# Kernel tuning notes

Measured on AMD Instinct MI355X. Metric: run time of the kernel, lower is better.

The kernel has to match this reference:

```python
import jax, jax.numpy as jnp
import numpy as np

H = 512      # hidden_size
NH = 8       # num_heads
DH = H // NH # head_dim = 64
NL = 2       # num_layers
R = 64       # number of AST relation types
PAD = 0      # padding relation index
FF = 4 * H   # FFN inner dim
B, T, S = 4, 512, 512
NEG = -1e10
EPS = 1e-5


def layer_norm(x, g, b):
    m = jnp.mean(x, axis=-1, keepdims=True)
    v = jnp.mean((x - m) ** 2, axis=-1, keepdims=True)
    return (x - m) * jax.lax.rsqrt(v + EPS) * g + b


def setup_inputs() -> dict:
    key = jax.random.key(0)
    ks = iter(jax.random.split(key, 40))

    def n(shape, scale=0.02):
        return jax.random.normal(next(ks), shape, dtype=jnp.float32) * scale

    inp = {
        'q': jax.random.normal(next(ks), (B, T, H), dtype=jnp.float32),
        'kv': jax.random.normal(next(ks), (B, S, H), dtype=jnp.float32),
        'rel_emb_k': n((R, DH)).at[PAD].set(0.0),
        'rel_emb_v': n((R, DH)).at[PAD].set(0.0),
        'Wq_s': n((NL, H, H)), 'bq_s': jnp.zeros((NL, H)),
        'Wk_s': n((NL, H, H)), 'Wv_s': n((NL, H, H)),
        'Wo_s': n((NL, H, H)), 'bo_s': jnp.zeros((NL, H)),
        'ln1_g': jnp.ones((NL, H)), 'ln1_b': jnp.zeros((NL, H)),
        'Wq_c': n((NL, H, H)), 'bq_c': jnp.zeros((NL, H)),
        'Wk_c': n((NL, H, H)), 'Wv_c': n((NL, H, H)),
        'Wo_c': n((NL, H, H)), 'bo_c': jnp.zeros((NL, H)),
        'ln2_g': jnp.ones((NL, H)), 'ln2_b': jnp.zeros((NL, H)),
        'W1': n((NL, H, FF)), 'b1': jnp.zeros((NL, FF)),
        'W2': n((NL, FF, H)), 'b2': jnp.zeros((NL, H)),
        'ln3_g': jnp.ones((NL, H)), 'ln3_b': jnp.zeros((NL, H)),
        'rel_ids': jax.random.randint(next(ks), (B, T, T), 0, R),
        'enc_mask': jnp.ones((B, S), dtype=bool),
    }
    return inp


def reference(q, kv, rel_emb_k, rel_emb_v,
              Wq_s, bq_s, Wk_s, Wv_s, Wo_s, bo_s, ln1_g, ln1_b,
              Wq_c, bq_c, Wk_c, Wv_c, Wo_c, bo_c, ln2_g, ln2_b,
              W1, b1, W2, b2, ln3_g, ln3_b,
              rel_ids, enc_mask):
    scale = np.sqrt(DH).astype(np.float32)
    # relation embeddings shared across layers/heads: [B,T,T,DH]
    rel_k = rel_emb_k[rel_ids]
    rel_v = rel_emb_v[rel_ids]
    tril = jnp.tril(jnp.ones((T, T), dtype=bool))
    rel_mask = (rel_ids != PAD) & tril[None]

    o = q
    for i in range(NL):
        # --- relation-aware masked self-attention ---
        Q = (o @ Wq_s[i] + bq_s[i]).reshape(B, T, NH, DH)
        K = (o @ Wk_s[i]).reshape(B, T, NH, DH)
        V = (o @ Wv_s[i]).reshape(B, T, NH, DH)
        # Q . (K + rel_k)^T decomposed to avoid materializing [B,NH,T,T,DH]
        e = (jnp.einsum('blhd,bmhd->bhlm', Q, K)
             + jnp.einsum('blhd,blmd->bhlm', Q, rel_k)) / scale
        e = jnp.where(rel_mask[:, None], e, NEG)
        a = jax.nn.softmax(e, axis=-1)
        att = (jnp.einsum('bhlm,bmhd->blhd', a, V)
               + jnp.einsum('bhlm,blmd->blhd', a, rel_v)).reshape(B, T, H)
        o = layer_norm(o + att @ Wo_s[i] + bo_s[i], ln1_g[i], ln1_b[i])

        # --- cross-attention ---
        Qc = (o @ Wq_c[i] + bq_c[i]).reshape(B, T, NH, DH)
        Kc = (kv @ Wk_c[i]).reshape(B, S, NH, DH)
        Vc = (kv @ Wv_c[i]).reshape(B, S, NH, DH)
        ec = jnp.einsum('bthd,bshd->bhts', Qc, Kc) / scale
        ec = jnp.where(enc_mask[:, None, None, :], ec, NEG)
        ac = jax.nn.softmax(ec, axis=-1)
        oc = jnp.einsum('bhts,bshd->bthd', ac, Vc).reshape(B, T, H)
        o = layer_norm(o + oc @ Wo_c[i] + bo_c[i], ln2_g[i], ln2_b[i])

        # --- feedforward ---
        h = jax.nn.relu(o @ W1[i] + b1[i])
        o = layer_norm(o + h @ W2[i] + b2[i], ln3_g[i], ln3_b[i])
    return o
```

## Files before the change

kernel.cpp:

```cpp
#include <hip/hip_runtime.h>

static constexpr int Hc  = 512;
static constexpr int NHc = 8;
static constexpr int DHc = 64;
static constexpr int NLc = 2;
static constexpr int Rc  = 64;
static constexpr int FFc = 2048;
static constexpr int Bc  = 4;
static constexpr int Tc  = 512;
#define NEGV (-1e10f)
#define EPSV 1e-5f
#define THRV 6.0f

typedef unsigned short u16;
typedef unsigned char u8;
typedef __attribute__((ext_vector_type(8))) short s16x8;
typedef __attribute__((ext_vector_type(4))) float f32x4;

__device__ __forceinline__ f32x4 mfma_bf16(s16x8 a, s16x8 b, f32x4 c) {
  return __builtin_amdgcn_mfma_f32_16x16x32_bf16(a, b, c, 0, 0, 0);
}
__device__ __forceinline__ u16 f2bf(float f) {
  union { float f; unsigned u; } x; x.f = f;
  unsigned r = (x.u + 0x7FFFu + ((x.u >> 16) & 1u)) >> 16;
  return (u16)r;
}
__device__ __forceinline__ float bf2f(u16 h) {
  union { unsigned u; float f; } x; x.u = ((unsigned)h) << 16;
  return x.f;
}
__device__ __forceinline__ unsigned cvtpk(float a, float b) {
  unsigned r;
  asm("v_cvt_pk_bf16_f32 %0, %1, %2" : "=v"(r) : "v"(a), "v"(b));
  return r;
}

template <int BM, int BN, bool RELU, int OUT>
__global__ __launch_bounds__(256) void gemm_mfma(
    const u16* __restrict__ A, const u16* __restrict__ Wt,
    const float* __restrict__ bias, int biasN,
    void* __restrict__ Cout, int N, int K) {
  __shared__ u16 As[BM * 32];
  __shared__ u16 Bs[BN * 32];
  const int tid = threadIdx.x;
  const int w = tid >> 6, lane = tid & 63, g = lane >> 4, li = lane & 15;
  const int bn = blockIdx.x * BN, bm = blockIdx.y * BM;
  const int r0 = (w & 1) * (BM / 2), c0 = (w >> 1) * (BN / 2);
  constexpr int MR = BM / 32, NR = BN / 32;
  constexpr int AIT = BM / 64, BIT = BN / 64;
  f32x4 acc[MR][NR];
#pragma unroll
  for (int i = 0; i < MR; ++i)
#pragma unroll
    for (int j = 0; j < NR; ++j) acc[i][j] = (f32x4){0.f, 0.f, 0.f, 0.f};

  s16x8 va[AIT], vb[BIT];
#pragma unroll
  for (int it = 0; it < AIT; ++it) {
    int s = it * 256 + tid, row = s >> 2, ch = s & 3;
    va[it] = *(const s16x8*)(A + (size_t)(bm + row) * K + ch * 8);
  }
#pragma unroll
  for (int it = 0; it < BIT; ++it) {
    int s = it * 256 + tid, row = s >> 2, ch = s & 3;
    vb[it] = *(const s16x8*)(Wt + (size_t)(bn + row) * K + ch * 8);
  }

  for (int k0 = 0; k0 < K; k0 += 32) {
    __syncthreads();
#pragma unroll
    for (int it = 0; it < AIT; ++it) {
      int s = it * 256 + tid, row = s >> 2, ch = s & 3;
      *(s16x8*)&As[row * 32 + ((ch ^ (row & 3)) * 8)] = va[it];
    }
#pragma unroll
    for (int it = 0; it < BIT; ++it) {
      int s = it * 256 + tid, row = s >> 2, ch = s & 3;
      *(s16x8*)&Bs[row * 32 + ((ch ^ (row & 3)) * 8)] = vb[it];
    }
    if (k0 + 32 < K) {
#pragma unroll
      for (int it = 0; it < AIT; ++it) {
        int s = it * 256 + tid, row = s >> 2, ch = s & 3;
        va[it] = *(const s16x8*)(A + (size_t)(bm + row) * K + k0 + 32 + ch * 8);
      }
#pragma unroll
      for (int it = 0; it < BIT; ++it) {
        int s = it * 256 + tid, row = s >> 2, ch = s & 3;
        vb[it] = *(const s16x8*)(Wt + (size_t)(bn + row) * K + k0 + 32 + ch * 8);
      }
    }
    __syncthreads();
    s16x8 ar[MR], br[NR];
#pragma unroll
    for (int i = 0; i < MR; ++i) {
      int row = r0 + i * 16 + li;
      ar[i] = *(const s16x8*)&As[row * 32 + ((g ^ (row & 3)) * 8)];
    }
#pragma unroll
    for (int j = 0; j < NR; ++j) {
      int row = c0 + j * 16 + li;
      br[j] = *(const s16x8*)&Bs[row * 32 + ((g ^ (row & 3)) * 8)];
    }
#pragma unroll
    for (int i = 0; i < MR; ++i)
#pragma unroll
      for (int j = 0; j < NR; ++j) acc[i][j] = mfma_bf16(ar[i], br[j], acc[i][j]);
  }

#pragma unroll
  for (int j = 0; j < NR; ++j) {
    int col = bn + c0 + j * 16 + li;
    float bv = (bias && col < biasN) ? bias[col] : 0.f;
#pragma unroll
    for (int i = 0; i < MR; ++i) {
#pragma unroll
      for (int r = 0; r < 4; ++r) {
        int rowg = bm + r0 + i * 16 + 4 * g + r;
        float v = acc[i][j][r] + bv;
        if (RELU) v = fmaxf(v, 0.f);
        if (OUT == 0) ((float*)Cout)[(size_t)rowg * N + col] = v;
        else          ((u16*)Cout)[(size_t)rowg * N + col] = f2bf(v);
      }
    }
  }
}

struct WPtrs { const float* p[10]; };

__global__ __launch_bounds__(256) void wcvt(WPtrs wp, u16* __restrict__ dst) {
  constexpr int NE = 20;
  constexpr int srcIdx[NE] = {0,1,0,1,3,3,4,4,5,5,6,6,7,7,2,2,8,8,9,9};
  constexpr int srcOff[NE] = {0,0,262144,262144,0,262144,0,262144,0,262144,
                              0,262144,0,262144,0,262144,0,1048576,0,1048576};
  constexpr int dstOff[NE] = {0,262144,524288,786432,1048576,1310720,
                              1572864,1835008,2097152,2359296,2621440,2883584,
                              3145728,3407872,3670016,3932160,
                              4194304,5242880,6291456,7340032};
  constexpr int KsA[NE] = {512,512,512,512,512,512,512,512,512,512,
                           512,512,512,512,512,512,512,512,2048,2048};
  constexpr int NsA[NE] = {512,512,512,512,512,512,512,512,512,512,
                           512,512,512,512,512,512,2048,2048,512,512};
  constexpr int tileStart[NE] = {0,64,128,192,256,320,384,448,512,576,
                                 640,704,768,832,896,960,1024,1280,1536,1792};
  __shared__ float ts[64 * 65];
  const int tid = threadIdx.x;
  const int bid = blockIdx.x;
  int e = 0;
#pragma unroll
  for (int i = 1; i < NE; ++i) if (bid >= tileStart[i]) e = i;
  const int t = bid - tileStart[e];
  const int Ks_ = KsA[e], Ns_ = NsA[e];
  const int tn = t % (Ns_ >> 6), tk = t / (Ns_ >> 6);
  const float* src = wp.p[srcIdx[e]] + srcOff[e];

  {
    int r = tid >> 2, cb = (tid & 3) * 16;
    const float* sp = src + (size_t)(tk * 64 + r) * Ns_ + tn * 64 + cb;
#pragma unroll
    for (int j = 0; j < 4; ++j) {
      float4 v = ((const float4*)sp)[j];
      float* d = &ts[r * 65 + cb + j * 4];
      d[0] = v.x; d[1] = v.y; d[2] = v.z; d[3] = v.w;
    }
  }
  __syncthreads();
  {
    int n = tid >> 2, kb = (tid & 3) * 16;
    u16* dp = dst + dstOff[e] + (size_t)(tn * 64 + n) * Ks_ + tk * 64 + kb;
    s16x8 o0, o1;
#pragma unroll
    for (int j = 0; j < 8; ++j) o0[j] = (short)f2bf(ts[(kb + j) * 65 + n]);
#pragma unroll
    for (int j = 0; j < 8; ++j) o1[j] = (short)f2bf(ts[(kb + 8 + j) * 65 + n]);
    *(s16x8*)dp = o0;
    *(s16x8*)(dp + 8) = o1;
  }
}

__global__ __launch_bounds__(256) void acvt(
    const float* __restrict__ q, const float* __restrict__ kv,
    const float* __restrict__ relv, const int* __restrict__ rel,
    u16* __restrict__ obf, u16* __restrict__ kvbf, u16* __restrict__ relvt,
    u8* __restrict__ rel8, float* __restrict__ ocp) {
  int bid = blockIdx.x, tid = threadIdx.x;
  if (bid >= 1025) {
    size_t i = (size_t)(bid - 1025) * 2048 + (size_t)tid * 8;
    int4 a = *(const int4*)(rel + i);
    int4 b = *(const int4*)(rel + i + 4);
    unsigned lo = (unsigned)(a.x & 255) | ((unsigned)(a.y & 255) << 8) |
                  ((unsigned)(a.z & 255) << 16) | ((unsigned)(a.w & 255) << 24);
    unsigned hi = (unsigned)(b.x & 255) | ((unsigned)(b.y & 255) << 8) |
                  ((unsigned)(b.z & 255) << 16) | ((unsigned)(b.w & 255) << 24);
    *(uint2*)(rel8 + i) = make_uint2(lo, hi);
    return;
  }
  if (bid == 1024) {
    int d = tid >> 2, rb = (tid & 3) * 16;
    s16x8 o0, o1;
#pragma unroll
    for (int j = 0; j < 8; ++j) o0[j] = (short)f2bf(relv[(rb + j) * 64 + d]);
#pragma unroll
    for (int j = 0; j < 8; ++j) o1[j] = (short)f2bf(relv[(rb + 8 + j) * 64 + d]);
    *(s16x8*)(relvt + d * 64 + rb) = o0;
    *(s16x8*)(relvt + d * 64 + rb + 8) = o1;
    return;
  }
  int i = bid * 256 + tid;
  const float* src; u16* dst; size_t off;
  bool isq = (i < 131072);
  if (isq) { src = q; dst = obf; off = (size_t)i * 8; }
  else { src = kv; dst = kvbf; off = (size_t)(i - 131072) * 8; }
  float4 a = *(const float4*)(src + off);
  float4 b = *(const float4*)(src + off + 4);
  if (isq) {
    *(float4*)(ocp + off) = a;
    *(float4*)(ocp + off + 4) = b;
  }
  s16x8 o;
  o[0] = (short)f2bf(a.x); o[1] = (short)f2bf(a.y);
  o[2] = (short)f2bf(a.z); o[3] = (short)f2bf(a.w);
  o[4] = (short)f2bf(b.x); o[5] = (short)f2bf(b.y);
  o[6] = (short)f2bf(b.z); o[7] = (short)f2bf(b.w);
  *(s16x8*)(dst + off) = o;
}

__global__ __launch_bounds__(256) void qr_kernel(
    const u16* __restrict__ Q, const float* __restrict__ relk,
    u16* __restrict__ Qr) {
  __shared__ float rk[64 * 65];
  __shared__ float qs[4][64];
  const int tid = threadIdx.x;
  {
    int r = tid >> 2, cb = (tid & 3) * 16;
    const float* sp = relk + r * 64 + cb;
#pragma unroll
    for (int j = 0; j < 4; ++j) {
      float4 v = ((const float4*)sp)[j];
      float* d = &rk[r * 65 + cb + j * 4];
      d[0] = v.x; d[1] = v.y; d[2] = v.z; d[3] = v.w;
    }
  }
  const int sub = tid >> 6, r = tid & 63;
  const int unit = blockIdx.x * 4 + sub;
  qs[sub][r] = bf2f(Q[(size_t)(unit >> 3) * 1024 + (unit & 7) * 64 + r]);
  __syncthreads();
  float acc = 0.f;
#pragma unroll
  for (int d = 0; d < 64; ++d) acc += qs[sub][d] * rk[r * 65 + d];
  Qr[(size_t)unit * 64 + r] = f2bf(acc);
}

__global__ __launch_bounds__(128) void pack_frags(
    const u16* __restrict__ Kin, int kstride,
    const u16* __restrict__ VTin, int vstride,
    u16* __restrict__ Kf, u16* __restrict__ Vf) {
  const int t = threadIdx.x;
  const int c8 = blockIdx.x, h = blockIdx.y, b = blockIdx.z;
  u16* kdst = Kf + (size_t)((b * 8 + h) * 8 + c8) * 4096;
  u16* vdst = Vf + (size_t)((b * 8 + h) * 8 + c8) * 4096;
#pragma unroll
  for (int i = 0; i < 4; ++i) {
    int s = i * 128 + t;
    int mt = s >> 7, kk = (s >> 6) & 1, lane = s & 63;
    int g = lane >> 4, li = lane & 15;
    s16x8 kv = *(const s16x8*)(
        Kin + (size_t)(b * 512 + c8 * 64 + mt * 16 + li) * kstride +
        h * 64 + kk * 32 + g * 8);
    s16x8 vv = *(const s16x8*)(
        VTin + (size_t)(h * 64 + mt * 16 + li) * vstride +
        b * 512 + c8 * 64 + kk * 32 + g * 8);
    *(s16x8*)(kdst + (mt * 2 + kk) * 512 + lane * 8) = kv;
    *(s16x8*)(vdst + (mt * 2 + kk) * 512 + lane * 8) = vv;
  }
}

#define LOADKREL(KF, RF, C8) do {                                              \
    _Pragma("unroll") for (int mt = 0; mt < 4; ++mt) {                         \
      KF[mt * 2 + 0] = *(const s16x8*)(kfb + (size_t)(C8) * 4096 + (mt * 2 + 0) * 512 + lane * 8); \
      KF[mt * 2 + 1] = *(const s16x8*)(kfb + (size_t)(C8) * 4096 + (mt * 2 + 1) * 512 + lane * 8); \
      RF[mt] = *(const unsigned*)(rp8 + (C8) * 64 + mt * 16);                  \
    } } while (0)

#define COMPUTE_SELF(KF, RF, C8) do {                                          \
    s16x8 vf[8];                                                               \
    _Pragma("unroll") for (int df = 0; df < 4; ++df) {                         \
      vf[df * 2 + 0] = *(const s16x8*)(vfb + (size_t)(C8) * 4096 + (df * 2 + 0) * 512 + lane * 8); \
      vf[df * 2 + 1] = *(const s16x8*)(vfb + (size_t)(C8) * 4096 + (df * 2 + 1) * 512 + lane * 8); } \
    f32x4 sf[4];                                                               \
    _Pragma("unroll") for (int mt = 0; mt < 4; ++mt) {                         \
      sf[mt] = (f32x4){0.f, 0.f, 0.f, 0.f};                                    \
      sf[mt] = mfma_bf16(KF[mt * 2 + 0], aq0, sf[mt]);                         \
      sf[mt] = mfma_bf16(KF[mt * 2 + 1], aq1, sf[mt]); }                       \
    float p[4][4];                                                             \
    int rl[4][4];                                                              \
    float pmax = NEGV;                                                         \
    _Pragma("unroll") for (int mt = 0; mt < 4; ++mt) {                         \
      _Pragma("unroll") for (int r = 0; r < 4; ++r) {                          \
        int rel = (int)((RF[mt] >> (8 * r)) & 255u);                           \
        rl[mt][r] = rel;                                                       \
        bool valid = (rel != 0) && ((C8) * 64 + mt * 16 + 4 * g + r <= lrow);  \
        p[mt][r] = valid ? (sf[mt][r] + qrs[li * 66 + rel]) * 0.125f : NEGV;   \
        pmax = fmaxf(pmax, p[mt][r]); } }                                      \
    pmax = fmaxf(pmax, __shfl_xor(pmax, 16));                                  \
    pmax = fmaxf(pmax, __shfl_xor(pmax, 32));                                  \
    if (__any(pmax > mrow + THRV)) {                                           \
      float mnew = (pmax > mrow + THRV) ? pmax : mrow;                         \
      float f = __expf(mrow - mnew);                                           \
      rsum *= f;                                                               \
      _Pragma("unroll") for (int j = 0; j < 8; ++j) {                          \
        float2* p2 = (float2*)&bk[li * 66 + g * 16 + 2 * j];                   \
        float2 v = *p2; v.x *= f; v.y *= f; *p2 = v; }                         \
      _Pragma("unroll") for (int r = 0; r < 4; ++r) {                          \
        float fr = __shfl(f, 4 * g + r);                                       \
        _Pragma("unroll") for (int df = 0; df < 4; ++df) oacc[df][r] *= fr; }  \
      mrow = mnew; }                                                           \
    unsigned pk[4][2];                                                         \
    _Pragma("unroll") for (int mt = 0; mt < 4; ++mt) {                         \
      _Pragma("unroll") for (int r = 0; r < 4; ++r) {                          \
        float pv = __expf(p[mt][r] - mrow);                                    \
        p[mt][r] = pv;                                                         \
        rsum += pv;                                                            \
        if (pv > 0.f) atomicAdd(&bk[li * 66 + rl[mt][r]], pv); }               \
      pk[mt][0] = cvtpk(p[mt][0], p[mt][1]);                                   \
      pk[mt][1] = cvtpk(p[mt][2], p[mt][3]); }                                 \
    _Pragma("unroll") for (int kk = 0; kk < 2; ++kk) {                         \
      union { s16x8 v; unsigned u[4]; } pa;                                    \
      _Pragma("unroll") for (int q = 0; q < 4; ++q) {                          \
        int src = ((2 * (g & 1) + (q >> 1)) << 4) + li;                        \
        unsigned uA = __shfl(pk[2 * kk][q & 1], src);                          \
        unsigned uB = __shfl(pk[2 * kk + 1][q & 1], src);                      \
        pa.u[q] = (g < 2) ? uA : uB; }                                         \
      _Pragma("unroll") for (int df = 0; df < 4; ++df)                         \
        oacc[df] = mfma_bf16(pa.v, vf[df * 2 + kk], oacc[df]); }               \
  } while (0)

__global__ __launch_bounds__(64) void attn_self_part(
    const u16* __restrict__ Qb,
    const u16* __restrict__ Kf, const u16* __restrict__ Vf,
    const u16* __restrict__ Qrb, const u8* __restrict__ rel8,
    const u16* __restrict__ relvt,
    u16* __restrict__ po, float2* __restrict__ pms) {
  __shared__ float qrs[16 * 66];
  __shared__ float buck[16 * 66];
  float* bk = buck;

  const int lane = threadIdx.x;
  const int g = lane >> 4, li = lane & 15;
  const int qt = blockIdx.x, h = blockIdx.y;
  const int b = blockIdx.z >> 3, s = blockIdx.z & 7;
  const int lrow = qt * 16 + li;
  const int growq = b * 512 + qt * 16;

  const u16* qp = Qb + (size_t)(growq + li) * 1024 + h * 64;
  s16x8 aq0 = *(const s16x8*)(qp + g * 8);
  s16x8 aq1 = *(const s16x8*)(qp + 32 + g * 8);
  const u16* kfb = Kf + (size_t)((b * 8 + h) * 8) * 4096;
  const u16* vfb = Vf + (size_t)((b * 8 + h) * 8) * 4096;
  const u8* rp8 = rel8 + (size_t)(growq + li) * 512 + 4 * g;

  {
    int row = lane >> 2, c16 = (lane & 3) * 16;
    const u16* qrp = Qrb + ((size_t)(growq + row) * 8 + h) * 64 + c16;
    s16x8 v0 = *(const s16x8*)qrp;
    s16x8 v1 = *(const s16x8*)(qrp + 8);
#pragma unroll
    for (int j = 0; j < 8; ++j) {
      qrs[row * 66 + c16 + j] = bf2f((u16)v0[j]);
      qrs[row * 66 + c16 + 8 + j] = bf2f((u16)v1[j]);
    }
#pragma unroll
    for (int j = 0; j < 5; ++j) {
      int fid = j * 64 + lane;
      if (fid < 264) *(float4*)&buck[fid * 4] = make_float4(0.f, 0.f, 0.f, 0.f);
    }
  }

  float mrow = NEGV, rsum = 0.f;
  f32x4 oacc[4];
#pragma unroll
  for (int d = 0; d < 4; ++d) oacc[d] = (f32x4){0.f, 0.f, 0.f, 0.f};

  {
    s16x8 kA[8];
    unsigned rA[4];
    LOADKREL(kA, rA, s);
    COMPUTE_SELF(kA, rA, s);
  }

  rsum += __shfl_xor(rsum, 16);
  rsum += __shfl_xor(rsum, 32);

#pragma unroll
  for (int kk = 0; kk < 2; ++kk) {
    float bb[8];
#pragma unroll
    for (int j = 0; j < 4; ++j) {
      float2 v = *(const float2*)&bk[li * 66 + kk * 32 + g * 8 + 2 * j];
      bb[2 * j] = v.x; bb[2 * j + 1] = v.y;
    }
    union { s16x8 v; unsigned u[4]; } pb;
#pragma unroll
    for (int q = 0; q < 4; ++q) pb.u[q] = cvtpk(bb[2 * q], bb[2 * q + 1]);
#pragma unroll
    for (int df = 0; df < 4; ++df) {
      s16x8 rb = *(const s16x8*)(relvt + (df * 16 + li) * 64 + kk * 32 + g * 8);
      oacc[df] = mfma_bf16(pb.v, rb, oacc[df]);
    }
  }

  const size_t idx = (size_t)(b * 8 + h) * 512 + qt * 16;
#pragma unroll
  for (int df = 0; df < 4; ++df)
#pragma unroll
    for (int r = 0; r < 4; ++r)
      po[(idx + 4 * g + r) * 512 + s * 64 + df * 16 + li] = f2bf(oacc[df][r]);
  if (lane < 16) pms[(idx + lane) * 8 + s] = make_float2(mrow, rsum);
}

#define LOADK_X(KF, C8) do {                                                   \
    _Pragma("unroll") for (int mt = 0; mt < 4; ++mt) {                         \
      KF[mt * 2 + 0] = *(const s16x8*)(kfb + (size_t)(C8) * 4096 + (mt * 2 + 0) * 512 + lane * 8); \
      KF[mt * 2 + 1] = *(const s16x8*)(kfb + (size_t)(C8) * 4096 + (mt * 2 + 1) * 512 + lane * 8); \
    } } while (0)

#define COMPUTE_X(KF, C8) do {                                                 \
    s16x8 vf[8];                                                               \
    _Pragma("unroll") for (int df = 0; df < 4; ++df) {                         \
      vf[df * 2 + 0] = *(const s16x8*)(vfb + (size_t)(C8) * 4096 + (df * 2 + 0) * 512 + lane * 8); \
      vf[df * 2 + 1] = *(const s16x8*)(vfb + (size_t)(C8) * 4096 + (df * 2 + 1) * 512 + lane * 8); } \
    f32x4 sf[4];                                                               \
    _Pragma("unroll") for (int mt = 0; mt < 4; ++mt) {                         \
      sf[mt] = (f32x4){0.f, 0.f, 0.f, 0.f};                                    \
      sf[mt] = mfma_bf16(KF[mt * 2 + 0], aq0, sf[mt]);                         \
      sf[mt] = mfma_bf16(KF[mt * 2 + 1], aq1, sf[mt]); }                       \
    float p[4][4];                                                             \
    float pmax = NEGV;                                                         \
    _Pragma("unroll") for (int mt = 0; mt < 4; ++mt)                           \
      _Pragma("unroll") for (int r = 0; r < 4; ++r) {                          \
        p[mt][r] = sf[mt][r] * 0.125f;                                         \
        pmax = fmaxf(pmax, p[mt][r]); }                                        \
    pmax = fmaxf(pmax, __shfl_xor(pmax, 16));                                  \
    pmax = fmaxf(pmax, __shfl_xor(pmax, 32));                                  \
    if (__any(pmax > mrow + THRV)) {                                           \
      float mnew = (pmax > mrow + THRV) ? pmax : mrow;                         \
      float f = __expf(mrow - mnew);                                           \
      rsum *= f;                                                               \
      _Pragma("unroll") for (int r = 0; r < 4; ++r) {                          \
        float fr = __shfl(f, 4 * g + r);                                       \
        _Pragma("unroll") for (int df = 0; df < 4; ++df) oacc[df][r] *= fr; }  \
      mrow = mnew; }                                                           \
    unsigned pk[4][2];                                                         \
    _Pragma("unroll") for (int mt = 0; mt < 4; ++mt) {                         \
      _Pragma("unroll") for (int r = 0; r < 4; ++r) {                          \
        float pv = __expf(p[mt][r] - mrow);                                    \
        p[mt][r] = pv;                                                         \
        rsum += pv; }                                                          \
      pk[mt][0] = cvtpk(p[mt][0], p[mt][1]);                                   \
      pk[mt][1] = cvtpk(p[mt][2], p[mt][3]); }                                 \
    _Pragma("unroll") for (int kk = 0; kk < 2; ++kk) {                         \
      union { s16x8 v; unsigned u[4]; } pa;                                    \
      _Pragma("unroll") for (int q = 0; q < 4; ++q) {                          \
        int src = ((2 * (g & 1) + (q >> 1)) << 4) + li;                        \
        unsigned uA = __shfl(pk[2 * kk][q & 1], src);                          \
        unsigned uB = __shfl(pk[2 * kk + 1][q & 1], src);                      \
        pa.u[q] = (g < 2) ? uA : uB; }                                         \
      _Pragma("unroll") for (int df = 0; df < 4; ++df)                         \
        oacc[df] = mfma_bf16(pa.v, vf[df * 2 + kk], oacc[df]); }               \
  } while (0)

__global__ __launch_bounds__(64) void attn_cross_part(
    const u16* __restrict__ Qb,
    const u16* __restrict__ Kf, const u16* __restrict__ Vf,
    u16* __restrict__ po, float2* __restrict__ pms) {
  const int lane = threadIdx.x;
  const int g = lane >> 4, li = lane & 15;
  const int qt = blockIdx.x, h = blockIdx.y;
  const int b = blockIdx.z >> 3, s = blockIdx.z & 7;
  const int growq = b * 512 + qt * 16;

  const u16* qp = Qb + (size_t)(growq + li) * 512 + h * 64;
  s16x8 aq0 = *(const s16x8*)(qp + g * 8);
  s16x8 aq1 = *(const s16x8*)(qp + 32 + g * 8);
  const u16* kfb = Kf + (size_t)((b * 8 + h) * 8) * 4096;
  const u16* vfb = Vf + (size_t)((b * 8 + h) * 8) * 4096;

  float mrow = NEGV, rsum = 0.f;
  f32x4 oacc[4];
#pragma unroll
  for (int d = 0; d < 4; ++d) oacc[d] = (f32x4){0.f, 0.f, 0.f, 0.f};

  {
    s16x8 kA[8];
    LOADK_X(kA, s);
    COMPUTE_X(kA, s);
  }

  rsum += __shfl_xor(rsum, 16);
  rsum += __shfl_xor(rsum, 32);

  const size_t idx = (size_t)(b * 8 + h) * 512 + qt * 16;
#pragma unroll
  for (int df = 0; df < 4; ++df)
#pragma unroll
    for (int r = 0; r < 4; ++r)
      po[(idx + 4 * g + r) * 512 + s * 64 + df * 16 + li] = f2bf(oacc[df][r]);
  if (lane < 16) pms[(idx + lane) * 8 + s] = make_float2(mrow, rsum);
}

__global__ __launch_bounds__(256) void attn_merge(
    const u16* __restrict__ po, const float2* __restrict__ pms,
    u16* __restrict__ att) {
  const int t = threadIdx.x;
  const size_t idx = (size_t)blockIdx.x * 16 + (t >> 4);
  const int d4 = (t & 15) * 4;
  float2 ms[8];
  float m = NEGV;
#pragma unroll
  for (int s = 0; s < 8; ++s) {
    ms[s] = pms[idx * 8 + s];
    m = fmaxf(m, ms[s].x);
  }
  float rs = 0.f;
  float4 o = make_float4(0.f, 0.f, 0.f, 0.f);
#pragma unroll
  for (int s = 0; s < 8; ++s) {
    float f = __expf(ms[s].x - m);
    rs += f * ms[s].y;
    ushort4 v = *(const ushort4*)(po + idx * 512 + s * 64 + d4);
    o.x += f * bf2f(v.x); o.y += f * bf2f(v.y);
    o.z += f * bf2f(v.z); o.w += f * bf2f(v.w);
  }
  const float inv = 1.f / rs;
  const int b = (int)(idx >> 12), h = (int)(idx >> 9) & 7, row = (int)(idx & 511);
  ushort4 ov;
  ov.x = f2bf(o.x * inv);
  ov.y = f2bf(o.y * inv);
  ov.z = f2bf(o.z * inv);
  ov.w = f2bf(o.w * inv);
  *(ushort4*)(att + (size_t)(b * 512 + row) * 512 + h * 64 + d4) = ov;
}

__global__ __launch_bounds__(256) void ln_res(
    const float* __restrict__ x, const float* __restrict__ dlt,
    const float* __restrict__ g, const float* __restrict__ bta,
    float* __restrict__ out, u16* __restrict__ obf) {
  __shared__ float red_s[256];
  const int row = blockIdx.x, tid = threadIdx.x;
  const size_t base = (size_t)row * Hc;
  float v0 = x[base + tid] + dlt[base + tid];
  float v1 = x[base + tid + 256] + dlt[base + tid + 256];

  red_s[tid] = v0 + v1;
  __syncthreads();
  for (int s = 128; s > 0; s >>= 1) {
    if (tid < s) red_s[tid] += red_s[tid + s];
    __syncthreads();
  }
  const float mean = red_s[0] * (1.f / Hc);
  __syncthreads();
  const float d0 = v0 - mean, d1 = v1 - mean;
  red_s[tid] = d0 * d0 + d1 * d1;
  __syncthreads();
  for (int s = 128; s > 0; s >>= 1) {
    if (tid < s) red_s[tid] += red_s[tid + s];
    __syncthreads();
  }
  const float rstd = rsqrtf(red_s[0] * (1.f / Hc) + EPSV);
  float o0 = d0 * rstd * g[tid] + bta[tid];
  float o1 = d1 * rstd * g[tid + 256] + bta[tid + 256];
  out[base + tid] = o0;
  out[base + tid + 256] = o1;
  obf[base + tid] = f2bf(o0);
  obf[base + tid + 256] = f2bf(o1);
}

extern "C" void kernel_launch(void* const* d_in, const int* in_sizes, int n_in,
                              void* d_out, int out_size, void* d_ws, size_t ws_size,
                              hipStream_t stream) {
  const float* q    = (const float*)d_in[0];
  const float* kv   = (const float*)d_in[1];
  const float* relk = (const float*)d_in[2];
  const float* relv = (const float*)d_in[3];
  const float* Wq_s = (const float*)d_in[4];
  const float* bq_s = (const float*)d_in[5];
  const float* Wk_s = (const float*)d_in[6];
  const float* Wv_s = (const float*)d_in[7];
  const float* Wo_s = (const float*)d_in[8];
  const float* bo_s = (const float*)d_in[9];
  const float* ln1g = (const float*)d_in[10];
  const float* ln1b = (const float*)d_in[11];
  const float* Wq_c = (const float*)d_in[12];
  const float* bq_c = (const float*)d_in[13];
  const float* Wk_c = (const float*)d_in[14];
  const float* Wv_c = (const float*)d_in[15];
  const float* Wo_c = (const float*)d_in[16];
  const float* bo_c = (const float*)d_in[17];
  const float* ln2g = (const float*)d_in[18];
  const float* ln2b = (const float*)d_in[19];
  const float* W1   = (const float*)d_in[20];
  const float* b1   = (const float*)d_in[21];
  const float* W2   = (const float*)d_in[22];
  const float* b2   = (const float*)d_in[23];
  const float* ln3g = (const float*)d_in[24];
  const float* ln3b = (const float*)d_in[25];
  const int*   rel  = (const int*)d_in[26];

  char* wsb = (char*)d_ws;
  const size_t NT = (size_t)Bc * Tc;
  float* o     = (float*)wsb;  wsb += NT * Hc * 4;
  float* bDlt  = (float*)wsb;  wsb += NT * Hc * 4;
  u16* Qr      = (u16*)wsb;    wsb += NT * 8 * 64 * 2;
  u16* obf     = (u16*)wsb;    wsb += NT * Hc * 2;
  u16* kvbf    = (u16*)wsb;    wsb += NT * Hc * 2;
  u16* bQK     = (u16*)wsb;    wsb += NT * 1024 * 2;
  u16* bVt     = (u16*)wsb;    wsb += (size_t)512 * 2048 * 2;
  u16* bQc     = (u16*)wsb;    wsb += NT * Hc * 2;
  u16* bKc     = (u16*)wsb;    wsb += NT * 1024 * 2;
  u16* bVtc    = (u16*)wsb;    wsb += (size_t)1024 * 2048 * 2;
  u16* bAtt    = (u16*)wsb;    wsb += NT * Hc * 2;
  u16* bH      = (u16*)wsb;    wsb += NT * FFc * 2;
  u16* relvt   = (u16*)wsb;    wsb += 64 * 64 * 2;
  u8* rel8     = (u8*)wsb;     wsb += (size_t)NT * 512;
  u16* wbuf    = (u16*)wsb;    wsb += (size_t)8388608 * 2;
  u16* po      = (u16*)wsb;    wsb += (size_t)16384 * 512 * 2;
  float2* pms  = (float2*)wsb; wsb += (size_t)16384 * 8 * 8;
  u16* KfX0    = (u16*)wsb;    wsb += (size_t)1048576 * 2;
  u16* VfX0    = (u16*)wsb;    wsb += (size_t)1048576 * 2;
  u16* KfX1    = (u16*)wsb;    wsb += (size_t)1048576 * 2;
  u16* VfX1    = (u16*)wsb;    wsb += (size_t)1048576 * 2;
  u16* KfS     = bH;
  u16* VfS     = bH + 1048576;

  WPtrs wp;
  wp.p[0] = Wq_s; wp.p[1] = Wk_s; wp.p[2] = Wv_s; wp.p[3] = Wo_s;
  wp.p[4] = Wq_c; wp.p[5] = Wk_c; wp.p[6] = Wv_c; wp.p[7] = Wo_c;
  wp.p[8] = W1;   wp.p[9] = W2;

  dim3 blk(256);
  wcvt<<<dim3(2048), blk, 0, stream>>>(wp, wbuf);
  acvt<<<dim3(1537), blk, 0, stream>>>(q, kv, relv, rel, obf, kvbf, relvt,
                                       rel8, o);

  gemm_mfma<64, 128, false, 1><<<dim3(8, 32), blk, 0, stream>>>(
      kvbf, wbuf + 2097152, nullptr, 0, bKc, 1024, 512);
  gemm_mfma<64, 128, false, 1><<<dim3(16, 16), blk, 0, stream>>>(
      wbuf + 2621440, kvbf, nullptr, 0, bVtc, 2048, 512);
  const dim3 gPK(8, 8, 4);
  pack_frags<<<gPK, dim3(128), 0, stream>>>(bKc, 1024, bVtc, 2048, KfX0, VfX0);
  pack_frags<<<gPK, dim3(128), 0, stream>>>(bKc + 512, 1024,
      bVtc + (size_t)512 * 2048, 2048, KfX1, VfX1);

  const dim3 gLN(NT);
  const dim3 gPART(32, 8, 32);
  const dim3 gMERGE(1024);
  for (int i = 0; i < NLc; ++i) {
    gemm_mfma<64, 128, false, 1><<<dim3(8, 32), blk, 0, stream>>>(
        obf, wbuf + (size_t)i * 524288, bq_s + i * Hc, Hc, bQK, 1024, 512);
    gemm_mfma<64, 64, false, 1><<<dim3(32, 8), blk, 0, stream>>>(
        wbuf + 3670016 + (size_t)i * 262144, obf, nullptr, 0, bVt, 2048, 512);
    qr_kernel<<<dim3(4096), blk, 0, stream>>>(bQK, relk, Qr);
    pack_frags<<<gPK, dim3(128), 0, stream>>>(bQK + 512, 1024, bVt, 2048, KfS, VfS);
    attn_self_part<<<gPART, dim3(64), 0, stream>>>(
        bQK, KfS, VfS, Qr, rel8, relvt, po, pms);
    attn_merge<<<gMERGE, blk, 0, stream>>>(po, pms, bAtt);
    gemm_mfma<64, 64, false, 0><<<dim3(8, 32), blk, 0, stream>>>(
        bAtt, wbuf + 1048576 + (size_t)i * 262144, bo_s + i * Hc, Hc, bDlt, Hc, 512);
    ln_res<<<gLN, blk, 0, stream>>>(o, bDlt, ln1g + i * Hc, ln1b + i * Hc, o, obf);

    gemm_mfma<64, 64, false, 1><<<dim3(8, 32), blk, 0, stream>>>(
        obf, wbuf + 1572864 + (size_t)i * 262144, bq_c + i * Hc, Hc, bQc, Hc, 512);
    attn_cross_part<<<gPART, dim3(64), 0, stream>>>(
        bQc, i ? KfX1 : KfX0, i ? VfX1 : VfX0, po, pms);
    attn_merge<<<gMERGE, blk, 0, stream>>>(po, pms, bAtt);
    gemm_mfma<64, 64, false, 0><<<dim3(8, 32), blk, 0, stream>>>(
        bAtt, wbuf + 3145728 + (size_t)i * 262144, bo_c + i * Hc, Hc, bDlt, Hc, 512);
    ln_res<<<gLN, blk, 0, stream>>>(o, bDlt, ln2g + i * Hc, ln2b + i * Hc, o, obf);

    gemm_mfma<64, 128, true, 1><<<dim3(16, 32), blk, 0, stream>>>(
        obf, wbuf + 4194304 + (size_t)i * 1048576, b1 + i * FFc, FFc, bH, FFc, 512);
    gemm_mfma<64, 64, false, 0><<<dim3(8, 32), blk, 0, stream>>>(
        bH, wbuf + 6291456 + (size_t)i * 1048576, b2 + i * Hc, Hc, bDlt, Hc, 2048);
    float* lnout = (i == NLc - 1) ? (float*)d_out : o;
    ln_res<<<gLN, blk, 0, stream>>>(o, bDlt, ln3g + i * Hc, ln3b + i * Hc, lnout, obf);
  }
}
```

Measured before the change: 380.8 us.

## Drop split-KV attention partials and merge pass, fuse prep and pack kernels

Self- and cross-attention kernels now loop over all eight key chunks inside one block and normalise the output directly. This removes the partial-output and max/sum buffers and both attn_merge launches. The weight and activation conversion kernels are merged into one prep launch, qr_kernel is fused with the self-attention fragment packing, and the two cross-attention pack launches become one. The aim is to cut launch count and the round trip of partial results through memory. The cost is an 8x smaller attention grid of single-wave blocks, which leaves much less parallelism and latency hiding per CU.

New measurement: 366.5 us. 3.7% less time.

```diff
diff --git a/kernel.cpp b/kernel.cpp
--- a/kernel.cpp
+++ b/kernel.cpp
@@ -128,62 +128,63 @@
 
 struct WPtrs { const float* p[10]; };
 
-__global__ __launch_bounds__(256) void wcvt(WPtrs wp, u16* __restrict__ dst) {
-  constexpr int NE = 20;
-  constexpr int srcIdx[NE] = {0,1,0,1,3,3,4,4,5,5,6,6,7,7,2,2,8,8,9,9};
-  constexpr int srcOff[NE] = {0,0,262144,262144,0,262144,0,262144,0,262144,
-                              0,262144,0,262144,0,262144,0,1048576,0,1048576};
-  constexpr int dstOff[NE] = {0,262144,524288,786432,1048576,1310720,
-                              1572864,1835008,2097152,2359296,2621440,2883584,
-                              3145728,3407872,3670016,3932160,
-                              4194304,5242880,6291456,7340032};
-  constexpr int KsA[NE] = {512,512,512,512,512,512,512,512,512,512,
-                           512,512,512,512,512,512,512,512,2048,2048};
-  constexpr int NsA[NE] = {512,512,512,512,512,512,512,512,512,512,
-                           512,512,512,512,512,512,2048,2048,512,512};
-  constexpr int tileStart[NE] = {0,64,128,192,256,320,384,448,512,576,
-                                 640,704,768,832,896,960,1024,1280,1536,1792};
-  __shared__ float ts[64 * 65];
-  const int tid = threadIdx.x;
-  const int bid = blockIdx.x;
-  int e = 0;
-#pragma unroll
-  for (int i = 1; i < NE; ++i) if (bid >= tileStart[i]) e = i;
-  const int t = bid - tileStart[e];
-  const int Ks_ = KsA[e], Ns_ = NsA[e];
-  const int tn = t % (Ns_ >> 6), tk = t / (Ns_ >> 6);
-  const float* src = wp.p[srcIdx[e]] + srcOff[e];
-
-  {
-    int r = tid >> 2, cb = (tid & 3) * 16;
-    const float* sp = src + (size_t)(tk * 64 + r) * Ns_ + tn * 64 + cb;
-#pragma unroll
-    for (int j = 0; j < 4; ++j) {
-      float4 v = ((const float4*)sp)[j];
-      float* d = &ts[r * 65 + cb + j * 4];
-      d[0] = v.x; d[1] = v.y; d[2] = v.z; d[3] = v.w;
-    }
-  }
-  __syncthreads();
-  {
-    int n = tid >> 2, kb = (tid & 3) * 16;
-    u16* dp = dst + dstOff[e] + (size_t)(tn * 64 + n) * Ks_ + tk * 64 + kb;
-    s16x8 o0, o1;
-#pragma unroll
-    for (int j = 0; j < 8; ++j) o0[j] = (short)f2bf(ts[(kb + j) * 65 + n]);
-#pragma unroll
-    for (int j = 0; j < 8; ++j) o1[j] = (short)f2bf(ts[(kb + 8 + j) * 65 + n]);
-    *(s16x8*)dp = o0;
-    *(s16x8*)(dp + 8) = o1;
-  }
-}
-
-__global__ __launch_bounds__(256) void acvt(
+__global__ __launch_bounds__(256) void prep(
+    WPtrs wp, u16* __restrict__ dst,
     const float* __restrict__ q, const float* __restrict__ kv,
     const float* __restrict__ relv, const int* __restrict__ rel,
     u16* __restrict__ obf, u16* __restrict__ kvbf, u16* __restrict__ relvt,
     u8* __restrict__ rel8, float* __restrict__ ocp) {
-  int bid = blockIdx.x, tid = threadIdx.x;
+  __shared__ float ts[64 * 65];
+  const int tid = threadIdx.x;
+  const int bid0 = blockIdx.x;
+  if (bid0 < 2048) {
+    constexpr int NE = 20;
+    constexpr int srcIdx[NE] = {0,1,0,1,3,3,4,4,5,5,6,6,7,7,2,2,8,8,9,9};
+    constexpr int srcOff[NE] = {0,0,262144,262144,0,262144,0,262144,0,262144,
+                                0,262144,0,262144,0,262144,0,1048576,0,1048576};
+    constexpr int dstOff[NE] = {0,262144,524288,786432,1048576,1310720,
+                                1572864,1835008,2097152,2359296,2621440,2883584,
+                                3145728,3407872,3670016,3932160,
+                                4194304,5242880,6291456,7340032};
+    constexpr int KsA[NE] = {512,512,512,512,512,512,512,512,512,512,
+                             512,512,512,512,512,512,512,512,2048,2048};
+    constexpr int NsA[NE] = {512,512,512,512,512,512,512,512,512,512,
+                             512,512,512,512,512,512,2048,2048,512,512};
+    constexpr int tileStart[NE] = {0,64,128,192,256,320,384,448,512,576,
+                                   640,704,768,832,896,960,1024,1280,1536,1792};
+    const int bid = bid0;
+    int e = 0;
+#pragma unroll
+    for (int i = 1; i < NE; ++i) if (bid >= tileStart[i]) e = i;
+    const int t = bid - tileStart[e];
+    const int Ks_ = KsA[e], Ns_ = NsA[e];
+    const int tn = t % (Ns_ >> 6), tk = t / (Ns_ >> 6);
+    const float* src = wp.p[srcIdx[e]] + srcOff[e];
+    {
+      int r = tid >> 2, cb = (tid & 3) * 16;
+      const float* sp = src + (size_t)(tk * 64 + r) * Ns_ + tn * 64 + cb;
+#pragma unroll
+      for (int j = 0; j < 4; ++j) {
+        float4 v = ((const float4*)sp)[j];
+        float* d = &ts[r * 65 + cb + j * 4];
+        d[0] = v.x; d[1] = v.y; d[2] = v.z; d[3] = v.w;
+      }
+    }
+    __syncthreads();
+    {
+      int n = tid >> 2, kb = (tid & 3) * 16;
+      u16* dp = dst + dstOff[e] + (size_t)(tn * 64 + n) * Ks_ + tk * 64 + kb;
+      s16x8 o0, o1;
+#pragma unroll
+      for (int j = 0; j < 8; ++j) o0[j] = (short)f2bf(ts[(kb + j) * 65 + n]);
+#pragma unroll
+      for (int j = 0; j < 8; ++j) o1[j] = (short)f2bf(ts[(kb + 8 + j) * 65 + n]);
+      *(s16x8*)dp = o0;
+      *(s16x8*)(dp + 8) = o1;
+    }
+    return;
+  }
+  const int bid = bid0 - 2048;
   if (bid >= 1025) {
     size_t i = (size_t)(bid - 1025) * 2048 + (size_t)tid * 8;
     int4 a = *(const int4*)(rel + i);
@@ -207,10 +208,10 @@
     return;
   }
   int i = bid * 256 + tid;
-  const float* src; u16* dst; size_t off;
+  const float* src; u16* dsta; size_t off;
   bool isq = (i < 131072);
-  if (isq) { src = q; dst = obf; off = (size_t)i * 8; }
-  else { src = kv; dst = kvbf; off = (size_t)(i - 131072) * 8; }
+  if (isq) { src = q; dsta = obf; off = (size_t)i * 8; }
+  else { src = kv; dsta = kvbf; off = (size_t)(i - 131072) * 8; }
   float4 a = *(const float4*)(src + off);
   float4 b = *(const float4*)(src + off + 4);
   if (isq) {
@@ -222,15 +223,39 @@
   o[2] = (short)f2bf(a.z); o[3] = (short)f2bf(a.w);
   o[4] = (short)f2bf(b.x); o[5] = (short)f2bf(b.y);
   o[6] = (short)f2bf(b.z); o[7] = (short)f2bf(b.w);
-  *(s16x8*)(dst + off) = o;
-}
-
-__global__ __launch_bounds__(256) void qr_kernel(
+  *(s16x8*)(dsta + off) = o;
+}
+
+__global__ __launch_bounds__(256) void qrpack(
     const u16* __restrict__ Q, const float* __restrict__ relk,
-    u16* __restrict__ Qr) {
+    u16* __restrict__ Qr,
+    const u16* __restrict__ Kin, const u16* __restrict__ VTin,
+    u16* __restrict__ Kf, u16* __restrict__ Vf) {
+  const int tid = threadIdx.x;
+  const int bid0 = blockIdx.x;
+  if (bid0 >= 4096) {
+    const int pb = bid0 - 4096;
+    const int c8 = pb & 7, h = (pb >> 3) & 7, b = pb >> 6;
+    u16* kdst = Kf + (size_t)((b * 8 + h) * 8 + c8) * 4096;
+    u16* vdst = Vf + (size_t)((b * 8 + h) * 8 + c8) * 4096;
+#pragma unroll
+    for (int i = 0; i < 2; ++i) {
+      int s = i * 256 + tid;
+      int mt = s >> 7, kk = (s >> 6) & 1, lane = s & 63;
+      int g = lane >> 4, li = lane & 15;
+      s16x8 kv = *(const s16x8*)(
+          Kin + (size_t)(b * 512 + c8 * 64 + mt * 16 + li) * 1024 +
+          h * 64 + kk * 32 + g * 8);
+      s16x8 vv = *(const s16x8*)(
+          VTin + (size_t)(h * 64 + mt * 16 + li) * 2048 +
+          b * 512 + c8 * 64 + kk * 32 + g * 8);
+      *(s16x8*)(kdst + (mt * 2 + kk) * 512 + lane * 8) = kv;
+      *(s16x8*)(vdst + (mt * 2 + kk) * 512 + lane * 8) = vv;
+    }
+    return;
+  }
   __shared__ float rk[64 * 65];
   __shared__ float qs[4][64];
-  const int tid = threadIdx.x;
   {
     int r = tid >> 2, cb = (tid & 3) * 16;
     const float* sp = relk + r * 64 + cb;
@@ -242,7 +267,7 @@
     }
   }
   const int sub = tid >> 6, r = tid & 63;
-  const int unit = blockIdx.x * 4 + sub;
+  const int unit = bid0 * 4 + sub;
   qs[sub][r] = bf2f(Q[(size_t)(unit >> 3) * 1024 + (unit & 7) * 64 + r]);
   __syncthreads();
   float acc = 0.f;
@@ -251,24 +276,27 @@
   Qr[(size_t)unit * 64 + r] = f2bf(acc);
 }
 
-__global__ __launch_bounds__(128) void pack_frags(
-    const u16* __restrict__ Kin, int kstride,
-    const u16* __restrict__ VTin, int vstride,
-    u16* __restrict__ Kf, u16* __restrict__ Vf) {
+__global__ __launch_bounds__(128) void pack_cross(
+    const u16* __restrict__ Kc,
+    const u16* __restrict__ VTc,
+    u16* __restrict__ Kf0, u16* __restrict__ Vf0) {
   const int t = threadIdx.x;
-  const int c8 = blockIdx.x, h = blockIdx.y, b = blockIdx.z;
-  u16* kdst = Kf + (size_t)((b * 8 + h) * 8 + c8) * 4096;
-  u16* vdst = Vf + (size_t)((b * 8 + h) * 8 + c8) * 4096;
+  const int c8 = blockIdx.x, h = blockIdx.y;
+  const int lay = blockIdx.z >> 2, b = blockIdx.z & 3;
+  const u16* Kin = Kc + lay * 512;
+  const u16* VTin = VTc + (size_t)lay * 512 * 2048;
+  u16* kdst = Kf0 + (size_t)lay * 2097152 + (size_t)((b * 8 + h) * 8 + c8) * 4096;
+  u16* vdst = Vf0 + (size_t)lay * 2097152 + (size_t)((b * 8 + h) * 8 + c8) * 4096;
 #pragma unroll
   for (int i = 0; i < 4; ++i) {
     int s = i * 128 + t;
     int mt = s >> 7, kk = (s >> 6) & 1, lane = s & 63;
     int g = lane >> 4, li = lane & 15;
     s16x8 kv = *(const s16x8*)(
-        Kin + (size_t)(b * 512 + c8 * 64 + mt * 16 + li) * kstride +
+        Kin + (size_t)(b * 512 + c8 * 64 + mt * 16 + li) * 1024 +
         h * 64 + kk * 32 + g * 8);
     s16x8 vv = *(const s16x8*)(
-        VTin + (size_t)(h * 64 + mt * 16 + li) * vstride +
+        VTin + (size_t)(h * 64 + mt * 16 + li) * 2048 +
         b * 512 + c8 * 64 + kk * 32 + g * 8);
     *(s16x8*)(kdst + (mt * 2 + kk) * 512 + lane * 8) = kv;
     *(s16x8*)(vdst + (mt * 2 + kk) * 512 + lane * 8) = vv;
@@ -335,20 +363,18 @@
         oacc[df] = mfma_bf16(pa.v, vf[df * 2 + kk], oacc[df]); }               \
   } while (0)
 
-__global__ __launch_bounds__(64) void attn_self_part(
+__global__ __launch_bounds__(64) void attn_self(
     const u16* __restrict__ Qb,
     const u16* __restrict__ Kf, const u16* __restrict__ Vf,
     const u16* __restrict__ Qrb, const u8* __restrict__ rel8,
-    const u16* __restrict__ relvt,
-    u16* __restrict__ po, float2* __restrict__ pms) {
+    const u16* __restrict__ relvt, u16* __restrict__ att) {
   __shared__ float qrs[16 * 66];
   __shared__ float buck[16 * 66];
   float* bk = buck;
 
   const int lane = threadIdx.x;
   const int g = lane >> 4, li = lane & 15;
-  const int qt = blockIdx.x, h = blockIdx.y;
-  const int b = blockIdx.z >> 3, s = blockIdx.z & 7;
+  const int qt = blockIdx.x, h = blockIdx.y, b = blockIdx.z;
   const int lrow = qt * 16 + li;
   const int growq = b * 512 + qt * 16;
 
@@ -381,11 +407,11 @@
 #pragma unroll
   for (int d = 0; d < 4; ++d) oacc[d] = (f32x4){0.f, 0.f, 0.f, 0.f};
 
-  {
+  for (int c = 0; c < 8; ++c) {
     s16x8 kA[8];
     unsigned rA[4];
-    LOADKREL(kA, rA, s);
-    COMPUTE_SELF(kA, rA, s);
+    LOADKREL(kA, rA, c);
+    COMPUTE_SELF(kA, rA, c);
   }
 
   rsum += __shfl_xor(rsum, 16);
@@ -409,13 +435,15 @@
     }
   }
 
-  const size_t idx = (size_t)(b * 8 + h) * 512 + qt * 16;
+  float inv[4];
+#pragma unroll
+  for (int r = 0; r < 4; ++r) inv[r] = 1.f / __shfl(rsum, 4 * g + r);
 #pragma unroll
   for (int df = 0; df < 4; ++df)
 #pragma unroll
     for (int r = 0; r < 4; ++r)
-      po[(idx + 4 * g + r) * 512 + s * 64 + df * 16 + li] = f2bf(oacc[df][r]);
-  if (lane < 16) pms[(idx + lane) * 8 + s] = make_float2(mrow, rsum);
+      att[(size_t)(growq + 4 * g + r) * 512 + h * 64 + df * 16 + li] =
+          f2bf(oacc[df][r] * inv[r]);
 }
 
 #define LOADK_X(KF, C8) do {                                                   \
@@ -469,14 +497,13 @@
         oacc[df] = mfma_bf16(pa.v, vf[df * 2 + kk], oacc[df]); }               \
   } while (0)
 
-__global__ __launch_bounds__(64) void attn_cross_part(
+__global__ __launch_bounds__(64) void attn_cross(
     const u16* __restrict__ Qb,
     const u16* __restrict__ Kf, const u16* __restrict__ Vf,
-    u16* __restrict__ po, float2* __restrict__ pms) {
+    u16* __restrict__ att) {
   const int lane = threadIdx.x;
   const int g = lane >> 4, li = lane & 15;
-  const int qt = blockIdx.x, h = blockIdx.y;
-  const int b = blockIdx.z >> 3, s = blockIdx.z & 7;
+  const int qt = blockIdx.x, h = blockIdx.y, b = blockIdx.z;
   const int growq = b * 512 + qt * 16;
 
   const u16* qp = Qb + (size_t)(growq + li) * 512 + h * 64;
@@ -490,55 +517,23 @@
 #pragma unroll
   for (int d = 0; d < 4; ++d) oacc[d] = (f32x4){0.f, 0.f, 0.f, 0.f};
 
-  {
+  for (int c = 0; c < 8; ++c) {
     s16x8 kA[8];
-    LOADK_X(kA, s);
-    COMPUTE_X(kA, s);
+    LOADK_X(kA, c);
+    COMPUTE_X(kA, c);
   }
 
   rsum += __shfl_xor(rsum, 16);
   rsum += __shfl_xor(rsum, 32);
-
-  const size_t idx = (size_t)(b * 8 + h) * 512 + qt * 16;
+  float inv[4];
+#pragma unroll
+  for (int r = 0; r < 4; ++r) inv[r] = 1.f / __shfl(rsum, 4 * g + r);
 #pragma unroll
   for (int df = 0; df < 4; ++df)
 #pragma unroll
     for (int r = 0; r < 4; ++r)
-      po[(idx + 4 * g + r) * 512 + s * 64 + df * 16 + li] = f2bf(oacc[df][r]);
-  if (lane < 16) pms[(idx + lane) * 8 + s] = make_float2(mrow, rsum);
-}
-
-__global__ __launch_bounds__(256) void attn_merge(
-    const u16* __restrict__ po, const float2* __restrict__ pms,
-    u16* __restrict__ att) {
-  const int t = threadIdx.x;
-  const size_t idx = (size_t)blockIdx.x * 16 + (t >> 4);
-  const int d4 = (t & 15) * 4;
-  float2 ms[8];
-  float m = NEGV;
-#pragma unroll
-  for (int s = 0; s < 8; ++s) {
-    ms[s] = pms[idx * 8 + s];
-    m = fmaxf(m, ms[s].x);
-  }
-  float rs = 0.f;
-  float4 o = make_float4(0.f, 0.f, 0.f, 0.f);
-#pragma unroll
-  for (int s = 0; s < 8; ++s) {
-    float f = __expf(ms[s].x - m);
-    rs += f * ms[s].y;
-    ushort4 v = *(const ushort4*)(po + idx * 512 + s * 64 + d4);
-    o.x += f * bf2f(v.x); o.y += f * bf2f(v.y);
-    o.z += f * bf2f(v.z); o.w += f * bf2f(v.w);
-  }
-  const float inv = 1.f / rs;
-  const int b = (int)(idx >> 12), h = (int)(idx >> 9) & 7, row = (int)(idx & 511);
-  ushort4 ov;
-  ov.x = f2bf(o.x * inv);
-  ov.y = f2bf(o.y * inv);
-  ov.z = f2bf(o.z * inv);
-  ov.w = f2bf(o.w * inv);
-  *(ushort4*)(att + (size_t)(b * 512 + row) * 512 + h * 64 + d4) = ov;
+      att[(size_t)(growq + 4 * g + r) * 512 + h * 64 + df * 16 + li] =
+          f2bf(oacc[df][r] * inv[r]);
 }
 
 __global__ __launch_bounds__(256) void ln_res(
@@ -623,8 +618,6 @@
   u16* relvt   = (u16*)wsb;    wsb += 64 * 64 * 2;
   u8* rel8     = (u8*)wsb;     wsb += (size_t)NT * 512;
   u16* wbuf    = (u16*)wsb;    wsb += (size_t)8388608 * 2;
-  u16* po      = (u16*)wsb;    wsb += (size_t)16384 * 512 * 2;
-  float2* pms  = (float2*)wsb; wsb += (size_t)16384 * 8 * 8;
   u16* KfX0    = (u16*)wsb;    wsb += (size_t)1048576 * 2;
   u16* VfX0    = (u16*)wsb;    wsb += (size_t)1048576 * 2;
   u16* KfX1    = (u16*)wsb;    wsb += (size_t)1048576 * 2;
@@ -638,41 +631,34 @@
   wp.p[8] = W1;   wp.p[9] = W2;
 
   dim3 blk(256);
-  wcvt<<<dim3(2048), blk, 0, stream>>>(wp, wbuf);
-  acvt<<<dim3(1537), blk, 0, stream>>>(q, kv, relv, rel, obf, kvbf, relvt,
-                                       rel8, o);
+  prep<<<dim3(3585), blk, 0, stream>>>(wp, wbuf, q, kv, relv, rel,
+                                       obf, kvbf, relvt, rel8, o);
 
   gemm_mfma<64, 128, false, 1><<<dim3(8, 32), blk, 0, stream>>>(
       kvbf, wbuf + 2097152, nullptr, 0, bKc, 1024, 512);
   gemm_mfma<64, 128, false, 1><<<dim3(16, 16), blk, 0, stream>>>(
       wbuf + 2621440, kvbf, nullptr, 0, bVtc, 2048, 512);
-  const dim3 gPK(8, 8, 4);
-  pack_frags<<<gPK, dim3(128), 0, stream>>>(bKc, 1024, bVtc, 2048, KfX0, VfX0);
-  pack_frags<<<gPK, dim3(128), 0, stream>>>(bKc + 512, 1024,
-      bVtc + (size_t)512 * 2048, 2048, KfX1, VfX1);
+  pack_cross<<<dim3(8, 8, 8), dim3(128), 0, stream>>>(bKc, bVtc, KfX0, VfX0);
 
   const dim3 gLN(NT);
-  const dim3 gPART(32, 8, 32);
-  const dim3 gMERGE(1024);
+  const dim3 gATT(32, 8, 4);
   for (int i = 0; i < NLc; ++i) {
     gemm_mfma<64, 128, false, 1><<<dim3(8, 32), blk, 0, stream>>>(
         obf, wbuf + (size_t)i * 524288, bq_s + i * Hc, Hc, bQK, 1024, 512);
     gemm_mfma<64, 64, false, 1><<<dim3(32, 8), blk, 0, stream>>>(
         wbuf + 3670016 + (size_t)i * 262144, obf, nullptr, 0, bVt, 2048, 512);
-    qr_kernel<<<dim3(4096), blk, 0, stream>>>(bQK, relk, Qr);
-    pack_frags<<<gPK, dim3(128), 0, stream>>>(bQK + 512, 1024, bVt, 2048, KfS, VfS);
-    attn_self_part<<<gPART, dim3(64), 0, stream>>>(
-        bQK, KfS, VfS, Qr, rel8, relvt, po, pms);
-    attn_merge<<<gMERGE, blk, 0, stream>>>(po, pms, bAtt);
+    qrpack<<<dim3(4352), blk, 0, stream>>>(bQK, relk, Qr, bQK + 512, bVt,
+                                           KfS, VfS);
+    attn_self<<<gATT, dim3(64), 0, stream>>>(
+        bQK, KfS, VfS, Qr, rel8, relvt, bAtt);
     gemm_mfma<64, 64, false, 0><<<dim3(8, 32), blk, 0, stream>>>(
         bAtt, wbuf + 1048576 + (size_t)i * 262144, bo_s + i * Hc, Hc, bDlt, Hc, 512);
     ln_res<<<gLN, blk, 0, stream>>>(o, bDlt, ln1g + i * Hc, ln1b + i * Hc, o, obf);
 
     gemm_mfma<64, 64, false, 1><<<dim3(8, 32), blk, 0, stream>>>(
         obf, wbuf + 1572864 + (size_t)i * 262144, bq_c + i * Hc, Hc, bQc, Hc, 512);
-    attn_cross_part<<<gPART, dim3(64), 0, stream>>>(
-        bQc, i ? KfX1 : KfX0, i ? VfX1 : VfX0, po, pms);
-    attn_merge<<<gMERGE, blk, 0, stream>>>(po, pms, bAtt);
+    attn_cross<<<gATT, dim3(64), 0, stream>>>(
+        bQc, i ? (KfX0 + 2097152) : KfX0, i ? (VfX0 + 2097152) : VfX0, bAtt);
     gemm_mfma<64, 64, false, 0><<<dim3(8, 32), blk, 0, stream>>>(
         bAtt, wbuf + 3145728 + (size_t)i * 262144, bo_c + i * Hc, Hc, bDlt, Hc, 512);
     ln_res<<<gLN, blk, 0, stream>>>(o, bDlt, ln2g + i * Hc, ln2b + i * Hc, o, obf);
```
